# Optimization experiments

Measured on AMD Instinct MI355X. Metric: run time of the kernel, lower is better.

## Reference

```python
import jax, jax.numpy as jnp
import numpy as np

N_USERS = 100000
N_ITEMS = 50000
D = 64
N_LAYERS = 3
E_RAW = 2_000_000
B = 4096


def setup_inputs() -> dict:
    rng = np.random.RandomState(0)
    u = rng.randint(0, N_USERS, E_RAW).astype(np.int64)
    i = rng.randint(0, N_ITEMS, E_RAW).astype(np.int64)
    lin = np.unique(u * N_ITEMS + i)  # dedupe interactions like the dok_matrix would
    u = (lin // N_ITEMS).astype(np.int32)
    i = (lin % N_ITEMS).astype(np.int32)
    deg_u = np.bincount(u, minlength=N_USERS).astype(np.float64)
    deg_i = np.bincount(i, minlength=N_ITEMS).astype(np.float64)
    inv_u = np.where(deg_u > 0, 1.0 / np.sqrt(np.maximum(deg_u, 1.0)), 0.0)
    inv_i = np.where(deg_i > 0, 1.0 / np.sqrt(np.maximum(deg_i, 1.0)), 0.0)
    val = (inv_u[u] * inv_i[i]).astype(np.float32)  # D^-1/2 A D^-1/2 entries
    # symmetric bipartite Laplacian: user block rows then item block rows
    rows = np.concatenate([u, i + N_USERS]).astype(np.int32)
    cols = np.concatenate([i + N_USERS, u]).astype(np.int32)
    vals = np.concatenate([val, val])

    key = jax.random.key(0)
    k1, k2, k3, k4 = jax.random.split(key, 4)
    embeds = jax.random.normal(k1, (N_USERS + N_ITEMS, D), jnp.float32) * 0.1
    users = jax.random.randint(k2, (B,), 0, N_USERS)
    pos_items = jax.random.randint(k3, (B,), 0, N_ITEMS)
    neg_items = jax.random.randint(k4, (B,), 0, N_ITEMS)
    return dict(embeds=embeds, vals=jnp.asarray(vals), rows=jnp.asarray(rows),
                cols=jnp.asarray(cols), users=users, pos_items=pos_items,
                neg_items=neg_items)


def reference(embeds, vals, rows, cols, users, pos_items, neg_items):
    N = N_USERS + N_ITEMS
    cur = embeds
    acc = embeds  # running sum over layer embeddings (incl. layer 0)
    for _ in range(N_LAYERS):
        msg = vals[:, None] * cur[cols]                      # [nnz, D] gather
        cur = jax.ops.segment_sum(msg, rows, num_segments=N)  # SpMM scatter-add
        acc = acc + cur
    mean = acc / (N_LAYERS + 1)
    user_e = mean[:N_USERS]
    item_e = mean[N_USERS:]
    return user_e[users], item_e[pos_items], item_e[neg_items]
```

## Files before the change

kernel.cpp:

```cpp
#include <hip/hip_runtime.h>
#include <hip/hip_bf16.h>

#define N_USERS 100000
#define N_ITEMS 50000
#define N_TOT   150000
#define D       64
#define NBUCK   ((N_ITEMS + 255) >> 8)
#define BCAP    12288
#define CONVU_B 391
#define FLAG_B  48
#define SCAT_K  32

typedef float v2f __attribute__((ext_vector_type(2)));

__device__ __forceinline__ unsigned bf16rn(float f) {
    unsigned x = __float_as_uint(f);
    return (x + 0x7FFFu + ((x >> 16) & 1u)) >> 16;
}
__device__ __forceinline__ unsigned packbf(float a, float b) {
    return bf16rn(a) | (bf16rn(b) << 16);
}
__device__ __forceinline__ int lower_bound(const int* __restrict__ a, int n, int key) {
    int lo = 0, hi = n;
    while (lo < hi) {
        int mid = (lo + hi) >> 1;
        if (a[mid] < key) lo = mid + 1; else hi = mid;
    }
    return lo;
}

__global__ __launch_bounds__(256) void preA_kernel(
        const float* __restrict__ embeds, const int* __restrict__ rows,
        const int* __restrict__ cols, int* __restrict__ user_ptr,
        unsigned* __restrict__ ebfS, float* __restrict__ invrow,
        const int* __restrict__ users, const int* __restrict__ pos,
        const int* __restrict__ neg, unsigned char* __restrict__ flags,
        int* __restrict__ ccur, int* __restrict__ tmp,
        unsigned short* __restrict__ cols16, int E, int B) {
    int b = blockIdx.x, t = threadIdx.x;
    if (b < CONVU_B) {
        __shared__ int ptr_s[257];
        __shared__ float inv_s[256];
        int base = b * 256;
        int r = base + t;
        int v = lower_bound(rows, E, r);
        ptr_s[t] = v;
        if (r <= N_USERS) user_ptr[r] = v;
        if (t == 0) ptr_s[256] = lower_bound(rows, E, base + 256);
        __syncthreads();
        if (r < N_USERS) {
            int deg = ptr_s[t + 1] - ptr_s[t];
            float inv = (deg > 0) ? (float)(1.0 / sqrt((double)deg)) : 0.f;
            inv_s[t] = inv;
            invrow[r] = inv;
        } else inv_s[t] = 0.f;
        __syncthreads();
        int fl = t & 15;
        #pragma unroll
        for (int i = 0; i < 16; ++i) {
            int lr = i * 16 + (t >> 4);
            int row = base + lr;
            if (row < N_USERS) {
                float inv = inv_s[lr];
                float4 v4 = *(const float4*)(embeds + (size_t)row * D + fl * 4);
                uint2 o;
                o.x = packbf(inv * v4.x, inv * v4.y);
                o.y = packbf(inv * v4.z, inv * v4.w);
                *(uint2*)(ebfS + (size_t)row * 32 + fl * 2) = o;
            }
        }
    } else if (b < CONVU_B + FLAG_B) {
        int k = (b - CONVU_B) * 256 + t;
        if (k < 3 * B) {
            int row;
            if (k < B)          row = users[k];
            else if (k < 2 * B) row = N_USERS + pos[k - B];
            else                row = N_USERS + neg[k - 2 * B];
            flags[row] = 1;
        }
    } else {
        __shared__ int ebuf[256 * SCAT_K];
        __shared__ unsigned char bbuf[256 * SCAT_K];
        __shared__ int cnt[NBUCK];
        __shared__ int basep[NBUCK];
        int chunk = (b - CONVU_B - FLAG_B) * (256 * SCAT_K);
        if (t < NBUCK) cnt[t] = 0;
        __syncthreads();
        #pragma unroll 8
        for (int k = 0; k < SCAT_K; ++k) {
            int e = chunk + k * 256 + t;
            int idx = k * 256 + t;
            if (e < E) {
                int i = cols[e] - N_USERS;
                cols16[e] = (unsigned short)i;
                int bu = i >> 8;
                ebuf[idx] = ((i & 255) << 17) | rows[e];
                bbuf[idx] = (unsigned char)bu;
                atomicAdd(&cnt[bu], 1);
            } else bbuf[idx] = 255;
        }
        __syncthreads();
        if (t < NBUCK) {
            int c = cnt[t];
            basep[t] = c ? atomicAdd(&ccur[t], c) : 0;
            cnt[t] = 0;
        }
        __syncthreads();
        #pragma unroll 4
        for (int k = 0; k < SCAT_K; ++k) {
            int idx = k * 256 + t;
            int bu = bbuf[idx];
            if (bu < NBUCK) {
                int pos2 = basep[bu] + atomicAdd(&cnt[bu], 1);
                if (pos2 < BCAP)
                    tmp[(size_t)bu * BCAP + pos2] = ebuf[idx];
            }
        }
    }
}

__global__ __launch_bounds__(256) void preB_kernel(
        const int* __restrict__ tmp, const int* __restrict__ ccur,
        const float* __restrict__ embeds,
        int* __restrict__ item_beg, int* __restrict__ item_end,
        int* __restrict__ nbr, unsigned* __restrict__ ebfS,
        unsigned* __restrict__ bb1, float* __restrict__ invrow) {
    int b = blockIdx.x, t = threadIdx.x;
    if (b == NBUCK) {
        if (t < 16) {
            *(uint2*)(ebfS + (size_t)N_TOT * 32 + t * 2) = make_uint2(0u, 0u);
            *(uint2*)(bb1  + (size_t)N_TOT * 32 + t * 2) = make_uint2(0u, 0u);
        }
        if (t == 0) invrow[N_TOT] = 0.f;
        return;
    }
    __shared__ int stage[BCAP];
    __shared__ int hist[256];
    __shared__ int scn[256];
    __shared__ int curs[256];
    __shared__ float inv_s[256];
    int n = ccur[b]; if (n > BCAP) n = BCAP;
    const int* src = tmp + (size_t)b * BCAP;
    hist[t] = 0;
    __syncthreads();
    int n4 = n >> 2;
    const int4* src4 = (const int4*)src;
    for (int p = t; p < n4; p += 256) {
        int4 q = src4[p];
        *(int4*)(stage + p * 4) = q;
        atomicAdd(&hist[q.x >> 17], 1);
        atomicAdd(&hist[q.y >> 17], 1);
        atomicAdd(&hist[q.z >> 17], 1);
        atomicAdd(&hist[q.w >> 17], 1);
    }
    for (int p = (n4 << 2) + t; p < n; p += 256) {
        int q = src[p];
        stage[p] = q;
        atomicAdd(&hist[q >> 17], 1);
    }
    __syncthreads();
    scn[t] = hist[t];
    __syncthreads();
    for (int off = 1; off < 256; off <<= 1) {
        int x = (t >= off) ? scn[t - off] : 0;
        __syncthreads();
        scn[t] += x;
        __syncthreads();
    }
    {
        int excl = scn[t] - hist[t];
        curs[t] = excl;
        int gi = (b << 8) + t;
        float inv = (hist[t] > 0) ? (float)(1.0 / sqrt((double)hist[t])) : 0.f;
        inv_s[t] = inv;
        if (gi < N_ITEMS) {
            item_beg[gi] = b * BCAP + excl;
            item_end[gi] = b * BCAP + excl + hist[t];
            invrow[N_USERS + gi] = inv;
        }
    }
    __syncthreads();
    int* dst = nbr + (size_t)b * BCAP;
    for (int p = t; p < n4; p += 256) {
        int4 q = *(const int4*)(stage + p * 4);
        int p0 = atomicAdd(&curs[q.x >> 17], 1); dst[p0] = q.x & 0x1FFFF;
        int p1 = atomicAdd(&curs[q.y >> 17], 1); dst[p1] = q.y & 0x1FFFF;
        int p2 = atomicAdd(&curs[q.z >> 17], 1); dst[p2] = q.z & 0x1FFFF;
        int p3 = atomicAdd(&curs[q.w >> 17], 1); dst[p3] = q.w & 0x1FFFF;
    }
    for (int p = (n4 << 2) + t; p < n; p += 256) {
        int q = stage[p];
        int pos = atomicAdd(&curs[q >> 17], 1);
        dst[pos] = q & 0x1FFFF;
    }
    int fl = t & 15;
    #pragma unroll
    for (int i = 0; i < 16; ++i) {
        int lr = i * 16 + (t >> 4);
        int gi = (b << 8) + lr;
        if (gi < N_ITEMS) {
            int row = N_USERS + gi;
            float inv = inv_s[lr];
            float4 v4 = *(const float4*)(embeds + (size_t)row * D + fl * 4);
            uint2 o;
            o.x = packbf(inv * v4.x, inv * v4.y);
            o.y = packbf(inv * v4.z, inv * v4.w);
            *(uint2*)(ebfS + (size_t)row * 32 + fl * 2) = o;
        }
    }
}

__global__ __launch_bounds__(256) void agg_kernel(
        const unsigned* __restrict__ gsrc,
        float* __restrict__ nxt, unsigned* __restrict__ nxtb,
        const float* __restrict__ invrow,
        const unsigned char* __restrict__ flags,
        const int* __restrict__ user_ptr, const unsigned short* __restrict__ cols16,
        const int* __restrict__ item_beg, const int* __restrict__ item_end,
        const int* __restrict__ nbr) {
    int wave = (int)((blockIdx.x * blockDim.x + threadIdx.x) >> 6);
    int lane = (int)(threadIdx.x & 63);
    if (wave >= N_TOT) return;
    int g  = lane >> 3;
    int fl = lane & 7;

    bool is_user = wave < N_USERS;
    int s, epos, dummy;
    const unsigned* sb;
    if (is_user) {
        s = user_ptr[wave]; epos = user_ptr[wave + 1];
        sb = gsrc + (size_t)N_USERS * 32; dummy = N_ITEMS;
    } else {
        int i = wave - N_USERS; s = item_beg[i]; epos = item_end[i];
        sb = gsrc; dummy = N_TOT;
    }

    v2f a0 = {0.f, 0.f}, a1 = {0.f, 0.f}, a2 = {0.f, 0.f}, a3 = {0.f, 0.f};

    for (int base = s; base < epos; base += 64) {
        int cnt = epos - base; if (cnt > 64) cnt = 64;
        int col = dummy;
        if (lane < cnt)
            col = is_user ? (int)cols16[base + lane] : nbr[base + lane];
        int tcount = (cnt + 7) >> 3;
        #pragma unroll 8
        for (int t = 0; t < tcount; ++t) {
            int c = __shfl(col, 8 * t + g);
            uint4 q = *(const uint4*)(sb + (size_t)c * 32 + fl * 4);
            v2f p0 = {__uint_as_float(q.x << 16), __uint_as_float(q.x & 0xFFFF0000u)};
            v2f p1 = {__uint_as_float(q.y << 16), __uint_as_float(q.y & 0xFFFF0000u)};
            v2f p2 = {__uint_as_float(q.z << 16), __uint_as_float(q.z & 0xFFFF0000u)};
            v2f p3 = {__uint_as_float(q.w << 16), __uint_as_float(q.w & 0xFFFF0000u)};
            a0 += p0; a1 += p1; a2 += p2; a3 += p3;
        }
    }
    float acc[8] = {a0.x, a0.y, a1.x, a1.y, a2.x, a2.y, a3.x, a3.y};
    #pragma unroll
    for (int j = 0; j < 8; ++j) {
        acc[j] += __shfl_xor(acc[j], 8);
        acc[j] += __shfl_xor(acc[j], 16);
        acc[j] += __shfl_xor(acc[j], 32);
    }
    if (lane < 8) {
        float inv = invrow[wave];
        float f[8];
        #pragma unroll
        for (int j = 0; j < 8; ++j) f[j] = inv * acc[j];
        uint4 o;
        o.x = packbf(inv * f[0], inv * f[1]); o.y = packbf(inv * f[2], inv * f[3]);
        o.z = packbf(inv * f[4], inv * f[5]); o.w = packbf(inv * f[6], inv * f[7]);
        *(uint4*)(nxtb + (size_t)wave * 32 + fl * 4) = o;
        if (flags[wave]) {
            size_t ro = (size_t)wave * D + fl * 8;
            *(float4*)(nxt + ro)     = make_float4(f[0], f[1], f[2], f[3]);
            *(float4*)(nxt + ro + 4) = make_float4(f[4], f[5], f[6], f[7]);
        }
    }
}

__global__ __launch_bounds__(256) void agg3_fused_kernel(
        const unsigned* __restrict__ gsrc,
        const float* __restrict__ e0, const float* __restrict__ e1,
        const float* __restrict__ e2, const float* __restrict__ invrow,
        const int* __restrict__ users, const int* __restrict__ pos,
        const int* __restrict__ neg,
        const int* __restrict__ user_ptr, const unsigned short* __restrict__ cols16,
        const int* __restrict__ item_beg, const int* __restrict__ item_end,
        const int* __restrict__ nbr,
        float* __restrict__ out, int B) {
    int slot = (int)((blockIdx.x * blockDim.x + threadIdx.x) >> 6);
    int lane = (int)(threadIdx.x & 63);
    if (slot >= 3 * B) return;
    int g  = lane >> 3;
    int fl = lane & 7;

    int row;
    if (slot < B)          row = users[slot];
    else if (slot < 2 * B) row = N_USERS + pos[slot - B];
    else                   row = N_USERS + neg[slot - 2 * B];

    bool is_user = row < N_USERS;
    int s, epos, dummy;
    const unsigned* sb;
    if (is_user) {
        s = user_ptr[row]; epos = user_ptr[row + 1];
        sb = gsrc + (size_t)N_USERS * 32; dummy = N_ITEMS;
    } else {
        int i = row - N_USERS; s = item_beg[i]; epos = item_end[i];
        sb = gsrc; dummy = N_TOT;
    }

    v2f a0 = {0.f, 0.f}, a1 = {0.f, 0.f}, a2 = {0.f, 0.f}, a3 = {0.f, 0.f};

    for (int base = s; base < epos; base += 64) {
        int cnt = epos - base; if (cnt > 64) cnt = 64;
        int col = dummy;
        if (lane < cnt)
            col = is_user ? (int)cols16[base + lane] : nbr[base + lane];
        int tcount = (cnt + 7) >> 3;
        #pragma unroll 8
        for (int t = 0; t < tcount; ++t) {
            int c = __shfl(col, 8 * t + g);
            uint4 q = *(const uint4*)(sb + (size_t)c * 32 + fl * 4);
            v2f p0 = {__uint_as_float(q.x << 16), __uint_as_float(q.x & 0xFFFF0000u)};
            v2f p1 = {__uint_as_float(q.y << 16), __uint_as_float(q.y & 0xFFFF0000u)};
            v2f p2 = {__uint_as_float(q.z << 16), __uint_as_float(q.z & 0xFFFF0000u)};
            v2f p3 = {__uint_as_float(q.w << 16), __uint_as_float(q.w & 0xFFFF0000u)};
            a0 += p0; a1 += p1; a2 += p2; a3 += p3;
        }
    }
    float acc[8] = {a0.x, a0.y, a1.x, a1.y, a2.x, a2.y, a3.x, a3.y};
    #pragma unroll
    for (int j = 0; j < 8; ++j) {
        acc[j] += __shfl_xor(acc[j], 8);
        acc[j] += __shfl_xor(acc[j], 16);
        acc[j] += __shfl_xor(acc[j], 32);
    }
    if (lane < 8) {
        float inv = invrow[row];
        size_t ro = (size_t)row * D + fl * 8;
        float4 x0 = *(const float4*)(e0 + ro), x1 = *(const float4*)(e0 + ro + 4);
        float4 y0 = *(const float4*)(e1 + ro), y1 = *(const float4*)(e1 + ro + 4);
        float4 z0 = *(const float4*)(e2 + ro), z1 = *(const float4*)(e2 + ro + 4);
        float4 r0, r1;
        r0.x = (x0.x + y0.x + z0.x + inv * acc[0]) * 0.25f;
        r0.y = (x0.y + y0.y + z0.y + inv * acc[1]) * 0.25f;
        r0.z = (x0.z + y0.z + z0.z + inv * acc[2]) * 0.25f;
        r0.w = (x0.w + y0.w + z0.w + inv * acc[3]) * 0.25f;
        r1.x = (x1.x + y1.x + z1.x + inv * acc[4]) * 0.25f;
        r1.y = (x1.y + y1.y + z1.y + inv * acc[5]) * 0.25f;
        r1.z = (x1.z + y1.z + z1.z + inv * acc[6]) * 0.25f;
        r1.w = (x1.w + y1.w + z1.w + inv * acc[7]) * 0.25f;
        size_t oo = (size_t)slot * D + fl * 8;
        *(float4*)(out + oo)     = r0;
        *(float4*)(out + oo + 4) = r1;
    }
}

extern "C" void kernel_launch(void* const* d_in, const int* in_sizes, int n_in,
                              void* d_out, int out_size, void* d_ws, size_t ws_size,
                              hipStream_t stream) {
    const float* embeds = (const float*)d_in[0];
    const int*   rows   = (const int*)d_in[2];
    const int*   cols   = (const int*)d_in[3];
    const int*   users  = (const int*)d_in[4];
    const int*   pos    = (const int*)d_in[5];
    const int*   neg    = (const int*)d_in[6];
    const int E2 = in_sizes[1];
    const int E  = E2 / 2;
    const int B  = in_sizes[4];

    char* ws = (char*)d_ws;
    size_t off = 0;
    auto alloc = [&](size_t bytes) { void* p = ws + off; off = (off + bytes + 255) & ~(size_t)255; return p; };
    float*    buf1     = (float*)   alloc((size_t)N_TOT * D * sizeof(float));
    float*    buf2     = (float*)   alloc((size_t)N_TOT * D * sizeof(float));
    unsigned* ebfS     = (unsigned*)alloc((size_t)(N_TOT + 1) * 32 * sizeof(unsigned));
    unsigned* bb1      = (unsigned*)alloc((size_t)(N_TOT + 1) * 32 * sizeof(unsigned));
    int*      nbr      = (int*)     alloc((size_t)NBUCK * BCAP * sizeof(int));
    unsigned short* cols16 = (unsigned short*)alloc((size_t)E * sizeof(unsigned short));
    int*      user_ptr = (int*)     alloc((size_t)(N_USERS + 1) * sizeof(int));
    int*      item_beg = (int*)     alloc((size_t)N_ITEMS * sizeof(int));
    int*      item_end = (int*)     alloc((size_t)N_ITEMS * sizeof(int));
    float*    invrow   = (float*)   alloc((size_t)(N_TOT + 1) * sizeof(float));
    int*      ccur     = (int*)     alloc((size_t)NBUCK * sizeof(int));
    unsigned char* flags = (unsigned char*)alloc((size_t)N_TOT);
    int*      tmp      = (int*)buf1;

    size_t zspan = ((char*)flags + N_TOT) - (char*)ccur;
    hipMemsetAsync(ccur, 0, zspan, stream);
    const int scatB = (E + 256 * SCAT_K - 1) / (256 * SCAT_K);
    preA_kernel<<<CONVU_B + FLAG_B + scatB, 256, 0, stream>>>(
        embeds, rows, cols, user_ptr, ebfS, invrow, users, pos, neg, flags,
        ccur, tmp, cols16, E, B);
    preB_kernel<<<NBUCK + 1, 256, 0, stream>>>(
        tmp, ccur, embeds, item_beg, item_end, nbr, ebfS, bb1, invrow);

    const int blocks = (N_TOT + 3) / 4;
    agg_kernel<<<blocks, 256, 0, stream>>>(ebfS, buf1, bb1, invrow, flags, user_ptr,
                                           cols16, item_beg, item_end, nbr);
    agg_kernel<<<blocks, 256, 0, stream>>>(bb1, buf2, ebfS, invrow, flags, user_ptr,
                                           cols16, item_beg, item_end, nbr);

    agg3_fused_kernel<<<(3 * B + 3) / 4, 256, 0, stream>>>(
        ebfS, embeds, buf1, buf2, invrow, users, pos, neg,
        user_ptr, cols16, item_beg, item_end, nbr, (float*)d_out, B);
}
```

Measured before the change: 323.2 us.

## Replace bucketed item CSR build with fixed-stride per-item adjacency via global atomics

The item-side neighbor list is no longer built by a two-pass bucket scatter plus a per-bucket shared-memory counting sort. Instead, each edge atomically bumps a per-item counter and writes its user index directly into a fixed 96-slot row for that item. preB now only computes item degree normalisation and converts embeddings, and the aggregation kernels read item ranges as i*STRIDE plus the count. This removes a sort pass and its scratch traffic, but it adds global atomic contention and a nondeterministic neighbor order. Any item with more than 96 neighbors is silently truncated, which is fine for this input (about 40 per item on average) but is not a general guarantee.

After: 428.8 us. 1.33x slower.

```diff
diff --git a/kernel.cpp b/kernel.cpp
--- a/kernel.cpp
+++ b/kernel.cpp
@@ -5,11 +5,11 @@
 #define N_ITEMS 50000
 #define N_TOT   150000
 #define D       64
-#define NBUCK   ((N_ITEMS + 255) >> 8)
-#define BCAP    12288
+#define STRIDE  96
 #define CONVU_B 391
 #define FLAG_B  48
-#define SCAT_K  32
+#define SCAT_K  8
+#define ICONV_B 196
 
 typedef float v2f __attribute__((ext_vector_type(2)));
 
@@ -35,7 +35,7 @@
         unsigned* __restrict__ ebfS, float* __restrict__ invrow,
         const int* __restrict__ users, const int* __restrict__ pos,
         const int* __restrict__ neg, unsigned char* __restrict__ flags,
-        int* __restrict__ ccur, int* __restrict__ tmp,
+        int* __restrict__ icnt, int* __restrict__ nbr,
         unsigned short* __restrict__ cols16, int E, int B) {
     int b = blockIdx.x, t = threadIdx.x;
     if (b < CONVU_B) {
@@ -79,54 +79,27 @@
             flags[row] = 1;
         }
     } else {
-        __shared__ int ebuf[256 * SCAT_K];
-        __shared__ unsigned char bbuf[256 * SCAT_K];
-        __shared__ int cnt[NBUCK];
-        __shared__ int basep[NBUCK];
-        int chunk = (b - CONVU_B - FLAG_B) * (256 * SCAT_K);
-        if (t < NBUCK) cnt[t] = 0;
-        __syncthreads();
-        #pragma unroll 8
+        int base = (b - CONVU_B - FLAG_B) * (256 * SCAT_K);
+        #pragma unroll
         for (int k = 0; k < SCAT_K; ++k) {
-            int e = chunk + k * 256 + t;
-            int idx = k * 256 + t;
+            int e = base + k * 256 + t;
             if (e < E) {
                 int i = cols[e] - N_USERS;
                 cols16[e] = (unsigned short)i;
-                int bu = i >> 8;
-                ebuf[idx] = ((i & 255) << 17) | rows[e];
-                bbuf[idx] = (unsigned char)bu;
-                atomicAdd(&cnt[bu], 1);
-            } else bbuf[idx] = 255;
-        }
-        __syncthreads();
-        if (t < NBUCK) {
-            int c = cnt[t];
-            basep[t] = c ? atomicAdd(&ccur[t], c) : 0;
-            cnt[t] = 0;
-        }
-        __syncthreads();
-        #pragma unroll 4
-        for (int k = 0; k < SCAT_K; ++k) {
-            int idx = k * 256 + t;
-            int bu = bbuf[idx];
-            if (bu < NBUCK) {
-                int pos2 = basep[bu] + atomicAdd(&cnt[bu], 1);
-                if (pos2 < BCAP)
-                    tmp[(size_t)bu * BCAP + pos2] = ebuf[idx];
+                int p = atomicAdd(&icnt[i], 1);
+                if (p < STRIDE)
+                    nbr[(size_t)i * STRIDE + p] = rows[e];
             }
         }
     }
 }
 
 __global__ __launch_bounds__(256) void preB_kernel(
-        const int* __restrict__ tmp, const int* __restrict__ ccur,
-        const float* __restrict__ embeds,
-        int* __restrict__ item_beg, int* __restrict__ item_end,
-        int* __restrict__ nbr, unsigned* __restrict__ ebfS,
-        unsigned* __restrict__ bb1, float* __restrict__ invrow) {
+        const int* __restrict__ icnt, const float* __restrict__ embeds,
+        unsigned* __restrict__ ebfS, unsigned* __restrict__ bb1,
+        float* __restrict__ invrow) {
     int b = blockIdx.x, t = threadIdx.x;
-    if (b == NBUCK) {
+    if (b == ICONV_B) {
         if (t < 16) {
             *(uint2*)(ebfS + (size_t)N_TOT * 32 + t * 2) = make_uint2(0u, 0u);
             *(uint2*)(bb1  + (size_t)N_TOT * 32 + t * 2) = make_uint2(0u, 0u);
@@ -134,77 +107,28 @@
         if (t == 0) invrow[N_TOT] = 0.f;
         return;
     }
-    __shared__ int stage[BCAP];
-    __shared__ int hist[256];
-    __shared__ int scn[256];
-    __shared__ int curs[256];
     __shared__ float inv_s[256];
-    int n = ccur[b]; if (n > BCAP) n = BCAP;
-    const int* src = tmp + (size_t)b * BCAP;
-    hist[t] = 0;
+    int gi = (b << 8) + t;
+    float inv = 0.f;
+    if (gi < N_ITEMS) {
+        int deg = icnt[gi];
+        inv = (deg > 0) ? (float)(1.0 / sqrt((double)deg)) : 0.f;
+        invrow[N_USERS + gi] = inv;
+    }
+    inv_s[t] = inv;
     __syncthreads();
-    int n4 = n >> 2;
-    const int4* src4 = (const int4*)src;
-    for (int p = t; p < n4; p += 256) {
-        int4 q = src4[p];
-        *(int4*)(stage + p * 4) = q;
-        atomicAdd(&hist[q.x >> 17], 1);
-        atomicAdd(&hist[q.y >> 17], 1);
-        atomicAdd(&hist[q.z >> 17], 1);
-        atomicAdd(&hist[q.w >> 17], 1);
-    }
-    for (int p = (n4 << 2) + t; p < n; p += 256) {
-        int q = src[p];
-        stage[p] = q;
-        atomicAdd(&hist[q >> 17], 1);
-    }
-    __syncthreads();
-    scn[t] = hist[t];
-    __syncthreads();
-    for (int off = 1; off < 256; off <<= 1) {
-        int x = (t >= off) ? scn[t - off] : 0;
-        __syncthreads();
-        scn[t] += x;
-        __syncthreads();
-    }
-    {
-        int excl = scn[t] - hist[t];
-        curs[t] = excl;
-        int gi = (b << 8) + t;
-        float inv = (hist[t] > 0) ? (float)(1.0 / sqrt((double)hist[t])) : 0.f;
-        inv_s[t] = inv;
-        if (gi < N_ITEMS) {
-            item_beg[gi] = b * BCAP + excl;
-            item_end[gi] = b * BCAP + excl + hist[t];
-            invrow[N_USERS + gi] = inv;
-        }
-    }
-    __syncthreads();
-    int* dst = nbr + (size_t)b * BCAP;
-    for (int p = t; p < n4; p += 256) {
-        int4 q = *(const int4*)(stage + p * 4);
-        int p0 = atomicAdd(&curs[q.x >> 17], 1); dst[p0] = q.x & 0x1FFFF;
-        int p1 = atomicAdd(&curs[q.y >> 17], 1); dst[p1] = q.y & 0x1FFFF;
-        int p2 = atomicAdd(&curs[q.z >> 17], 1); dst[p2] = q.z & 0x1FFFF;
-        int p3 = atomicAdd(&curs[q.w >> 17], 1); dst[p3] = q.w & 0x1FFFF;
-    }
-    for (int p = (n4 << 2) + t; p < n; p += 256) {
-        int q = stage[p];
-        int pos = atomicAdd(&curs[q >> 17], 1);
-        dst[pos] = q & 0x1FFFF;
-    }
     int fl = t & 15;
     #pragma unroll
     for (int i = 0; i < 16; ++i) {
         int lr = i * 16 + (t >> 4);
-        int gi = (b << 8) + lr;
-        if (gi < N_ITEMS) {
-            int row = N_USERS + gi;
-            float inv = inv_s[lr];
+        int g2 = (b << 8) + lr;
+        if (g2 < N_ITEMS) {
+            int row = N_USERS + g2;
+            float invv = inv_s[lr];
             float4 v4 = *(const float4*)(embeds + (size_t)row * D + fl * 4);
             uint2 o;
-            o.x = packbf(inv * v4.x, inv * v4.y);
-            o.y = packbf(inv * v4.z, inv * v4.w);
+            o.x = packbf(invv * v4.x, invv * v4.y);
+            o.y = packbf(invv * v4.z, invv * v4.w);
             *(uint2*)(ebfS + (size_t)row * 32 + fl * 2) = o;
         }
     }
@@ -216,8 +140,7 @@
         const float* __restrict__ invrow,
         const unsigned char* __restrict__ flags,
         const int* __restrict__ user_ptr, const unsigned short* __restrict__ cols16,
-        const int* __restrict__ item_beg, const int* __restrict__ item_end,
-        const int* __restrict__ nbr) {
+        const int* __restrict__ icnt, const int* __restrict__ nbr) {
     int wave = (int)((blockIdx.x * blockDim.x + threadIdx.x) >> 6);
     int lane = (int)(threadIdx.x & 63);
     if (wave >= N_TOT) return;
@@ -231,7 +154,9 @@
         s = user_ptr[wave]; epos = user_ptr[wave + 1];
         sb = gsrc + (size_t)N_USERS * 32; dummy = N_ITEMS;
     } else {
-        int i = wave - N_USERS; s = item_beg[i]; epos = item_end[i];
+        int i = wave - N_USERS;
+        int c = icnt[i]; if (c > STRIDE) c = STRIDE;
+        s = i * STRIDE; epos = s + c;
         sb = gsrc; dummy = N_TOT;
     }
 
@@ -285,8 +210,7 @@
         const int* __restrict__ users, const int* __restrict__ pos,
         const int* __restrict__ neg,
         const int* __restrict__ user_ptr, const unsigned short* __restrict__ cols16,
-        const int* __restrict__ item_beg, const int* __restrict__ item_end,
-        const int* __restrict__ nbr,
+        const int* __restrict__ icnt, const int* __restrict__ nbr,
         float* __restrict__ out, int B) {
     int slot = (int)((blockIdx.x * blockDim.x + threadIdx.x) >> 6);
     int lane = (int)(threadIdx.x & 63);
@@ -306,7 +230,9 @@
         s = user_ptr[row]; epos = user_ptr[row + 1];
         sb = gsrc + (size_t)N_USERS * 32; dummy = N_ITEMS;
     } else {
-        int i = row - N_USERS; s = item_beg[i]; epos = item_end[i];
+        int i = row - N_USERS;
+        int c = icnt[i]; if (c > STRIDE) c = STRIDE;
+        s = i * STRIDE; epos = s + c;
         sb = gsrc; dummy = N_TOT;
     }
 
@@ -377,32 +303,28 @@
     float*    buf2     = (float*)   alloc((size_t)N_TOT * D * sizeof(float));
     unsigned* ebfS     = (unsigned*)alloc((size_t)(N_TOT + 1) * 32 * sizeof(unsigned));
     unsigned* bb1      = (unsigned*)alloc((size_t)(N_TOT + 1) * 32 * sizeof(unsigned));
-    int*      nbr      = (int*)     alloc((size_t)NBUCK * BCAP * sizeof(int));
+    int*      nbr      = (int*)     alloc((size_t)N_ITEMS * STRIDE * sizeof(int));
     unsigned short* cols16 = (unsigned short*)alloc((size_t)E * sizeof(unsigned short));
     int*      user_ptr = (int*)     alloc((size_t)(N_USERS + 1) * sizeof(int));
-    int*      item_beg = (int*)     alloc((size_t)N_ITEMS * sizeof(int));
-    int*      item_end = (int*)     alloc((size_t)N_ITEMS * sizeof(int));
     float*    invrow   = (float*)   alloc((size_t)(N_TOT + 1) * sizeof(float));
-    int*      ccur     = (int*)     alloc((size_t)NBUCK * sizeof(int));
+    int*      icnt     = (int*)     alloc((size_t)N_ITEMS * sizeof(int));
     unsigned char* flags = (unsigned char*)alloc((size_t)N_TOT);
-    int*      tmp      = (int*)buf1;
-
-    size_t zspan = ((char*)flags + N_TOT) - (char*)ccur;
-    hipMemsetAsync(ccur, 0, zspan, stream);
+
+    size_t zspan = ((char*)flags + N_TOT) - (char*)icnt;
+    hipMemsetAsync(icnt, 0, zspan, stream);
     const int scatB = (E + 256 * SCAT_K - 1) / (256 * SCAT_K);
     preA_kernel<<<CONVU_B + FLAG_B + scatB, 256, 0, stream>>>(
         embeds, rows, cols, user_ptr, ebfS, invrow, users, pos, neg, flags,
-        ccur, tmp, cols16, E, B);
-    preB_kernel<<<NBUCK + 1, 256, 0, stream>>>(
-        tmp, ccur, embeds, item_beg, item_end, nbr, ebfS, bb1, invrow);
+        icnt, nbr, cols16, E, B);
+    preB_kernel<<<ICONV_B + 1, 256, 0, stream>>>(icnt, embeds, ebfS, bb1, invrow);
 
     const int blocks = (N_TOT + 3) / 4;
     agg_kernel<<<blocks, 256, 0, stream>>>(ebfS, buf1, bb1, invrow, flags, user_ptr,
-                                           cols16, item_beg, item_end, nbr);
+                                           cols16, icnt, nbr);
     agg_kernel<<<blocks, 256, 0, stream>>>(bb1, buf2, ebfS, invrow, flags, user_ptr,
-                                           cols16, item_beg, item_end, nbr);
+                                           cols16, icnt, nbr);
 
     agg3_fused_kernel<<<(3 * B + 3) / 4, 256, 0, stream>>>(
         ebfS, embeds, buf1, buf2, invrow, users, pos, neg,
-        user_ptr, cols16, item_beg, item_end, nbr, (float*)d_out, B);
-}
+        user_ptr, cols16, icnt, nbr, (float*)d_out, B);
+}
```

## Pack four rows per wavefront in SpMM aggregation kernel

Applied to the files above, without the earlier changes.

Changes the aggregation kernel so each 64-lane wave handles four rows (16 lanes per row, two neighbors per step) instead of one row per wave. User rows average about 20 neighbors and item rows about 40, so the one-row mapping left many lanes idle. The new mapping cuts the reduction shuffles and the grid size by four. The cost is that the four rows in a wave loop to the largest degree among them, so rows with uneven degrees cause lane divergence and some wasted iterations.

After: 292.6 us. -9.5%, faster.

```diff
diff --git a/kernel.cpp b/kernel.cpp
--- a/kernel.cpp
+++ b/kernel.cpp
@@ -220,58 +220,66 @@
         const int* __restrict__ nbr) {
     int wave = (int)((blockIdx.x * blockDim.x + threadIdx.x) >> 6);
     int lane = (int)(threadIdx.x & 63);
-    if (wave >= N_TOT) return;
-    int g  = lane >> 3;
-    int fl = lane & 7;
-
-    bool is_user = wave < N_USERS;
+    if (wave >= (N_TOT >> 2)) return;
+    int r  = lane >> 4;
+    int q  = lane & 15;
+    int g2 = q >> 3;
+    int fl = q & 7;
+
+    int row = (wave << 2) + r;
+    bool is_user = row < N_USERS;
     int s, epos, dummy;
     const unsigned* sb;
     if (is_user) {
-        s = user_ptr[wave]; epos = user_ptr[wave + 1];
+        s = user_ptr[row]; epos = user_ptr[row + 1];
         sb = gsrc + (size_t)N_USERS * 32; dummy = N_ITEMS;
     } else {
-        int i = wave - N_USERS; s = item_beg[i]; epos = item_end[i];
+        int i = row - N_USERS; s = item_beg[i]; epos = item_end[i];
         sb = gsrc; dummy = N_TOT;
     }
+    int deg = epos - s;
+    int mdeg = deg;
+    mdeg = max(mdeg, __shfl_xor(mdeg, 16));
+    mdeg = max(mdeg, __shfl_xor(mdeg, 32));
+    int nchunk = (mdeg + 15) >> 4;
 
     v2f a0 = {0.f, 0.f}, a1 = {0.f, 0.f}, a2 = {0.f, 0.f}, a3 = {0.f, 0.f};
 
-    for (int base = s; base < epos; base += 64) {
-        int cnt = epos - base; if (cnt > 64) cnt = 64;
+    for (int ch = 0; ch < nchunk; ++ch) {
+        int base = s + (ch << 4);
+        int cnt = epos - base;
+        if (cnt > 16) cnt = 16;
         int col = dummy;
-        if (lane < cnt)
-            col = is_user ? (int)cols16[base + lane] : nbr[base + lane];
-        int tcount = (cnt + 7) >> 3;
+        if (q < cnt)
+            col = is_user ? (int)cols16[base + q] : nbr[base + q];
+        int cm = mdeg - (ch << 4); if (cm > 16) cm = 16;
+        int tcm = (cm + 1) >> 1;
         #pragma unroll 8
-        for (int t = 0; t < tcount; ++t) {
-            int c = __shfl(col, 8 * t + g);
-            uint4 q = *(const uint4*)(sb + (size_t)c * 32 + fl * 4);
-            v2f p0 = {__uint_as_float(q.x << 16), __uint_as_float(q.x & 0xFFFF0000u)};
-            v2f p1 = {__uint_as_float(q.y << 16), __uint_as_float(q.y & 0xFFFF0000u)};
-            v2f p2 = {__uint_as_float(q.z << 16), __uint_as_float(q.z & 0xFFFF0000u)};
-            v2f p3 = {__uint_as_float(q.w << 16), __uint_as_float(q.w & 0xFFFF0000u)};
+        for (int t = 0; t < tcm; ++t) {
+            int c = __shfl(col, (r << 4) + 2 * t + g2);
+            uint4 qv = *(const uint4*)(sb + (size_t)c * 32 + fl * 4);
+            v2f p0 = {__uint_as_float(qv.x << 16), __uint_as_float(qv.x & 0xFFFF0000u)};
+            v2f p1 = {__uint_as_float(qv.y << 16), __uint_as_float(qv.y & 0xFFFF0000u)};
+            v2f p2 = {__uint_as_float(qv.z << 16), __uint_as_float(qv.z & 0xFFFF0000u)};
+            v2f p3 = {__uint_as_float(qv.w << 16), __uint_as_float(qv.w & 0xFFFF0000u)};
             a0 += p0; a1 += p1; a2 += p2; a3 += p3;
         }
     }
     float acc[8] = {a0.x, a0.y, a1.x, a1.y, a2.x, a2.y, a3.x, a3.y};
     #pragma unroll
-    for (int j = 0; j < 8; ++j) {
+    for (int j = 0; j < 8; ++j)
         acc[j] += __shfl_xor(acc[j], 8);
-        acc[j] += __shfl_xor(acc[j], 16);
-        acc[j] += __shfl_xor(acc[j], 32);
-    }
-    if (lane < 8) {
-        float inv = invrow[wave];
+    if (q < 8) {
+        float inv = invrow[row];
         float f[8];
         #pragma unroll
         for (int j = 0; j < 8; ++j) f[j] = inv * acc[j];
         uint4 o;
         o.x = packbf(inv * f[0], inv * f[1]); o.y = packbf(inv * f[2], inv * f[3]);
         o.z = packbf(inv * f[4], inv * f[5]); o.w = packbf(inv * f[6], inv * f[7]);
-        *(uint4*)(nxtb + (size_t)wave * 32 + fl * 4) = o;
-        if (flags[wave]) {
-            size_t ro = (size_t)wave * D + fl * 8;
+        *(uint4*)(nxtb + (size_t)row * 32 + fl * 4) = o;
+        if (flags[row]) {
+            size_t ro = (size_t)row * D + fl * 8;
             *(float4*)(nxt + ro)     = make_float4(f[0], f[1], f[2], f[3]);
             *(float4*)(nxt + ro + 4) = make_float4(f[4], f[5], f[6], f[7]);
         }
@@ -396,7 +404,7 @@
     preB_kernel<<<NBUCK + 1, 256, 0, stream>>>(
         tmp, ccur, embeds, item_beg, item_end, nbr, ebfS, bb1, invrow);
 
-    const int blocks = (N_TOT + 3) / 4;
+    const int blocks = N_TOT / 16;
     agg_kernel<<<blocks, 256, 0, stream>>>(ebfS, buf1, bb1, invrow, flags, user_ptr,
                                            cols16, item_beg, item_end, nbr);
     agg_kernel<<<blocks, 256, 0, stream>>>(bb1, buf2, ebfS, invrow, flags, user_ptr,
```
